# Kernel optimization log

Hardware: AMD Instinct MI355X
Metric: run time of the kernel (lower is better)

The kernel has to match this reference:

```python
import jax, jax.numpy as jnp
import numpy as np

B, S, D, H, DFF = 2, 2048, 1024, 16, 4096
DH = D // H
EPS = 1e-8


def _alibi_bias(num_heads, seq_len, dtype=jnp.float32):
    # ALiBi slopes for power-of-two head counts: 2^(-8*(h+1)/H)
    h = jnp.arange(1, num_heads + 1, dtype=dtype)
    slopes = jnp.exp2(-8.0 * h / num_heads)          # [H]
    pos = jnp.arange(seq_len, dtype=dtype)
    rel = jnp.abs(pos[None, :] - pos[:, None])       # [S, S] |i-j|
    return -slopes[:, None, None] * rel[None]        # [H, S, S]


def _rmsnorm(x, scale):
    rms = jax.lax.rsqrt(jnp.mean(x * x, axis=-1, keepdims=True) + EPS)
    return scale * x * rms


def setup_inputs() -> dict:
    key = jax.random.key(0)
    ks = jax.random.split(key, 12)
    sd = 0.02
    return {
        "x": jax.random.normal(ks[0], (B, S, D), jnp.float32),
        "scale1": jnp.ones((D,), jnp.float32),
        "scale2": jnp.ones((D,), jnp.float32),
        "w_qkv": jax.random.normal(ks[1], (D, 3 * D), jnp.float32) * sd,
        "b_qkv": jnp.zeros((3 * D,), jnp.float32),
        "w_out": jax.random.normal(ks[2], (D, D), jnp.float32) * sd,
        "b_out": jnp.zeros((D,), jnp.float32),
        "w1": jax.random.normal(ks[3], (D, DFF), jnp.float32) * sd,
        "b1": jnp.zeros((DFF,), jnp.float32),
        "w2": jax.random.normal(ks[4], (DFF, D), jnp.float32) * sd,
        "b2": jnp.zeros((D,), jnp.float32),
    }


def reference(x, scale1, scale2, w_qkv, b_qkv, w_out, b_out, w1, b1, w2, b2):
    residual = x
    xn = _rmsnorm(x, scale1)
    qkv = xn @ w_qkv + b_qkv                                  # [B,S,3D]
    q, k, v = jnp.split(qkv, 3, axis=-1)
    def heads(t):
        return t.reshape(B, S, H, DH).transpose(0, 2, 1, 3)   # [B,H,S,DH]
    q, k, v = heads(q), heads(k), heads(v)
    scores = jnp.einsum("bhsd,bhtd->bhst", q, k) / (DH ** 0.5)
    scores = scores + _alibi_bias(H, S, scores.dtype)[None]
    attn = jax.nn.softmax(scores, axis=-1)
    out = jnp.einsum("bhst,bhtd->bhsd", attn, v)              # [B,H,S,DH]
    out = out.transpose(0, 2, 1, 3).reshape(B, S, D)
    x = residual + (out @ w_out + b_out)
    residual = x
    xn = _rmsnorm(x, scale2)
    h = jax.nn.gelu(xn @ w1 + b1, approximate=False)
    return residual + (h @ w2 + b2)
```

## Files before the change

### kernel.cpp

```cpp
#include <hip/hip_runtime.h>
#include <hip/hip_bf16.h>
#include <math.h>

#define B_ 2
#define S_ 2048
#define D_ 1024
#define H_ 16
#define DH_ 64
#define DFF_ 4096
#define M_ (B_*S_)

typedef __bf16 bf16;
typedef __bf16 bf16x8 __attribute__((ext_vector_type(8)));
typedef __bf16 bf16x4 __attribute__((ext_vector_type(4)));
typedef float f32x4 __attribute__((ext_vector_type(4)));

__device__ __forceinline__ void gll16(const void* g, void* l) {
  __builtin_amdgcn_global_load_lds(
      (const __attribute__((address_space(1))) void*)g,
      (__attribute__((address_space(3))) void*)l, 16, 0, 0);
}

#define WAITCNT_VM4 0xF74
#define WAITCNT_VM0 0xF70

__global__ __launch_bounds__(256) void rmsnorm_kernel(const float* __restrict__ x,
    const float* __restrict__ scale, bf16* __restrict__ out) {
  __shared__ float red[4];
  int row = blockIdx.x, t = threadIdx.x;
  const float4* xr = (const float4*)(x + (size_t)row * D_);
  float4 v = xr[t];
  float ss = v.x*v.x + v.y*v.y + v.z*v.z + v.w*v.w;
  #pragma unroll
  for (int off = 32; off > 0; off >>= 1) ss += __shfl_down(ss, off, 64);
  if ((t & 63) == 0) red[t >> 6] = ss;
  __syncthreads();
  float tot = red[0] + red[1] + red[2] + red[3];
  float r = rsqrtf(tot * (1.0f / D_) + 1e-8f);
  float4 sc = ((const float4*)scale)[t];
  bf16x4 o;
  o[0] = (bf16)(v.x * sc.x * r);
  o[1] = (bf16)(v.y * sc.y * r);
  o[2] = (bf16)(v.z * sc.z * r);
  o[3] = (bf16)(v.w * sc.w * r);
  *(bf16x4*)(out + (size_t)row * D_ + t * 4) = o;
}

__global__ __launch_bounds__(256) void reduce_rms_kernel(
    const bf16* __restrict__ p0, const bf16* __restrict__ p1,
    const float* __restrict__ x, const float* __restrict__ bias,
    const float* __restrict__ scale, float* __restrict__ x2, bf16* __restrict__ xn2) {
  __shared__ float red[4];
  int row = blockIdx.x, t = threadIdx.x;
  float4 xv = ((const float4*)(x + (size_t)row * D_))[t];
  float4 bv = ((const float4*)bias)[t];
  bf16x4 a = *(const bf16x4*)(p0 + (size_t)row * D_ + t * 4);
  bf16x4 b = *(const bf16x4*)(p1 + (size_t)row * D_ + t * 4);
  float s0 = xv.x + bv.x + (float)a[0] + (float)b[0];
  float s1 = xv.y + bv.y + (float)a[1] + (float)b[1];
  float s2 = xv.z + bv.z + (float)a[2] + (float)b[2];
  float s3 = xv.w + bv.w + (float)a[3] + (float)b[3];
  float4 o; o.x = s0; o.y = s1; o.z = s2; o.w = s3;
  ((float4*)(x2 + (size_t)row * D_))[t] = o;
  float ss = s0*s0 + s1*s1 + s2*s2 + s3*s3;
  #pragma unroll
  for (int off = 32; off > 0; off >>= 1) ss += __shfl_down(ss, off, 64);
  if ((t & 63) == 0) red[t >> 6] = ss;
  __syncthreads();
  float tot = red[0] + red[1] + red[2] + red[3];
  float r = rsqrtf(tot * (1.0f / D_) + 1e-8f);
  float4 sc = ((const float4*)scale)[t];
  bf16x4 on;
  on[0] = (bf16)(s0 * sc.x * r);
  on[1] = (bf16)(s1 * sc.y * r);
  on[2] = (bf16)(s2 * sc.z * r);
  on[3] = (bf16)(s3 * sc.w * r);
  *(bf16x4*)(xn2 + (size_t)row * D_ + t * 4) = on;
}

__global__ __launch_bounds__(256) void reduce_out_kernel(
    const bf16* __restrict__ p0, const bf16* __restrict__ p1,
    const float* __restrict__ x2, const float* __restrict__ bias,
    float* __restrict__ dout) {
  int row = blockIdx.x, t = threadIdx.x;
  float4 xv = ((const float4*)(x2 + (size_t)row * D_))[t];
  float4 bv = ((const float4*)bias)[t];
  bf16x4 a = *(const bf16x4*)(p0 + (size_t)row * D_ + t * 4);
  bf16x4 b = *(const bf16x4*)(p1 + (size_t)row * D_ + t * 4);
  float4 o;
  o.x = xv.x + bv.x + (float)a[0] + (float)b[0];
  o.y = xv.y + bv.y + (float)a[1] + (float)b[1];
  o.z = xv.z + bv.z + (float)a[2] + (float)b[2];
  o.w = xv.w + bv.w + (float)a[3] + (float)b[3];
  ((float4*)(dout + (size_t)row * D_))[t] = o;
}

__global__ __launch_bounds__(256) void wtrans_kernel(const float* __restrict__ W,
    bf16* __restrict__ Wt, int K, int N) {
  __shared__ float tile[32][33];
  int n0 = blockIdx.x * 32, k0 = blockIdx.y * 32;
  int tx = threadIdx.x & 31, ty = threadIdx.x >> 5;
  #pragma unroll
  for (int i = 0; i < 4; i++)
    tile[ty + i*8][tx] = W[(size_t)(k0 + ty + i*8) * N + n0 + tx];
  __syncthreads();
  #pragma unroll
  for (int i = 0; i < 4; i++)
    Wt[(size_t)(n0 + ty + i*8) * K + k0 + tx] = (bf16)tile[tx][ty + i*8];
}

__global__ __launch_bounds__(256) void vtrans_kernel(const bf16* __restrict__ Vin,
    bf16* __restrict__ Vt) {
  __shared__ bf16 tile[32][34];
  size_t base = (size_t)blockIdx.z * (S_ * DH_);
  int s0 = blockIdx.x * 32, d0 = blockIdx.y * 32;
  int tx = threadIdx.x & 31, ty = threadIdx.x >> 5;
  #pragma unroll
  for (int i = 0; i < 4; i++)
    tile[ty + i*8][tx] = Vin[base + (size_t)(s0 + ty + i*8) * DH_ + d0 + tx];
  __syncthreads();
  #pragma unroll
  for (int i = 0; i < 4; i++)
    Vt[base + (size_t)(d0 + ty + i*8) * S_ + s0 + tx] = tile[tx][ty + i*8];
}

__device__ __forceinline__ float gelu_fast(float x) {
  float e = __builtin_amdgcn_exp2f(2.3022585093f * x * (1.0f + 0.044715f * x * x));
  return x * e / (1.0f + e);
}

template<int MODE>
__global__ __launch_bounds__(256) void gemm_kernel(
    const bf16* __restrict__ A, const bf16* __restrict__ Bt,
    const float* __restrict__ bias, void* __restrict__ outp, void* __restrict__ outp2,
    int M, int N, int K, int lda) {
  __shared__ __align__(16) bf16 As[3][128 * 32];
  __shared__ __align__(16) bf16 Bs[3][128 * 32];
  int t = threadIdx.x;
  int wave = t >> 6, lane = t & 63;
  int lm = lane & 15, lg = lane >> 4;
  int m0 = blockIdx.y * 128, n0 = blockIdx.x * 128;
  size_t koff = (size_t)blockIdx.z * K;
  int wm = (wave >> 1) * 64, wn = (wave & 1) * 64;
  f32x4 acc[4][4] = {};

  int srow = t >> 2, sslot = t & 3;
  int scol = (sslot ^ ((srow >> 1) & 3)) * 8;
  const bf16* Ag = A + (size_t)(m0 + srow) * lda + koff + scol;
  const bf16* Bg = Bt + (size_t)(n0 + srow) * lda + koff + scol;
  size_t half = (size_t)64 * lda;
  int rsw = (lm >> 1) & 3;
  int nk = K >> 5;

  gll16(Ag, As[0] + t * 8);
  gll16(Ag + half, As[0] + 2048 + t * 8);
  gll16(Bg, Bs[0] + t * 8);
  gll16(Bg + half, Bs[0] + 2048 + t * 8);
  if (nk > 1) {
    gll16(Ag + 32, As[1] + t * 8);
    gll16(Ag + 32 + half, As[1] + 2048 + t * 8);
    gll16(Bg + 32, Bs[1] + t * 8);
    gll16(Bg + 32 + half, Bs[1] + 2048 + t * 8);
  }

  int buf = 0;
  for (int j = 0; j < nk; ++j) {
    if (j + 1 < nk) __builtin_amdgcn_s_waitcnt(WAITCNT_VM4);
    else            __builtin_amdgcn_s_waitcnt(WAITCNT_VM0);
    __builtin_amdgcn_s_barrier();
    if (j + 2 < nk) {
      int k2 = (j + 2) << 5;
      int nbuf = buf + 2; if (nbuf >= 3) nbuf -= 3;
      bf16* Ad = As[nbuf];
      bf16* Bd = Bs[nbuf];
      gll16(Ag + k2, Ad + t * 8);
      gll16(Ag + k2 + half, Ad + 2048 + t * 8);
      gll16(Bg + k2, Bd + t * 8);
      gll16(Bg + k2 + half, Bd + 2048 + t * 8);
    }
    const bf16* Ab = As[buf];
    const bf16* Bb = Bs[buf];
    if (++buf == 3) buf = 0;
    bf16x8 af[4], bfr[4];
    #pragma unroll
    for (int i = 0; i < 4; i++)
      af[i] = *(const bf16x8*)(Ab + (wm + i * 16 + lm) * 32 + (lg ^ rsw) * 8);
    #pragma unroll
    for (int j2 = 0; j2 < 4; j2++)
      bfr[j2] = *(const bf16x8*)(Bb + (wn + j2 * 16 + lm) * 32 + (lg ^ rsw) * 8);
    #pragma unroll
    for (int i = 0; i < 4; i++)
      #pragma unroll
      for (int j2 = 0; j2 < 4; j2++)
        acc[i][j2] = __builtin_amdgcn_mfma_f32_16x16x32_bf16(af[i], bfr[j2], acc[i][j2], 0, 0, 0);
  }

  bf16* pout = (MODE == 5) ? ((blockIdx.z == 0) ? (bf16*)outp : (bf16*)outp2) : (bf16*)outp;

  #pragma unroll
  for (int i = 0; i < 4; i++) {
    int row = m0 + wm + i * 16 + lg * 4;
    #pragma unroll
    for (int j = 0; j < 4; j++) {
      int col = n0 + wn + j * 16 + lm;
      float bcol = (MODE == 5) ? 0.f : bias[col];
      #pragma unroll
      for (int r = 0; r < 4; r++) {
        float v = acc[i][j][r] + bcol;
        int rr = row + r;
        if (MODE == 0) {
          int which = col >> 10, d = col & 1023;
          int hh = d >> 6, dh = d & 63;
          int bb = rr >> 11, s = rr & 2047;
          ((bf16*)outp)[(size_t)which * ((size_t)B_*H_*S_*DH_) +
              ((size_t)(bb * H_ + hh) * S_ + s) * DH_ + dh] = (bf16)v;
        } else if (MODE == 2) {
          ((bf16*)outp)[(size_t)rr * N + col] = (bf16)gelu_fast(v);
        } else {
          pout[(size_t)rr * N + col] = (bf16)v;
        }
      }
    }
  }
}

#define PSTR 68
__global__ __launch_bounds__(256, 3) void attn_kernel(
    const bf16* __restrict__ q, const bf16* __restrict__ k,
    const bf16* __restrict__ vT, bf16* __restrict__ ao) {
  __shared__ __align__(16) bf16 Ks[2][64 * 64];
  __shared__ __align__(16) bf16 Vs[2][64 * 64];
  __shared__ __align__(16) bf16 Ps[4 * 16 * PSTR];
  int t = threadIdx.x, wave = t >> 6, lane = t & 63;
  int lm = lane & 15, lg = lane >> 4;
  int q0 = blockIdx.x * 64;
  int h = blockIdx.y, b = blockIdx.z;
  size_t base = (size_t)(b * H_ + h) * ((size_t)S_ * DH_);
  const bf16* Q = q + base;
  const bf16* K = k + base;
  const bf16* V = vT + base;
  const float LOG2E = 1.4426950408889634f;
  float sl2 = exp2f(-0.5f * (float)(h + 1)) * LOG2E;
  float nslope = -sl2;
  const float qscale = 0.125f * LOG2E;
  const float FMAX = 8.0f;

  int W = (int)(24.0f / sl2);
  int jlo = (q0 - W) >> 6; if (jlo < 0) jlo = 0;
  int jhi = ((q0 + 63 + W) >> 6) + 1; if (jhi > S_ / 64) jhi = S_ / 64;

  bf16x8 qf[2];
  #pragma unroll
  for (int h2 = 0; h2 < 2; h2++) {
    bf16x8 v = *(const bf16x8*)(Q + (size_t)(q0 + wave * 16 + lm) * DH_ + h2 * 32 + lg * 8);
    #pragma unroll
    for (int e = 0; e < 8; e++) v[e] = (bf16)((float)v[e] * qscale);
    qf[h2] = v;
  }

  int row0 = t >> 3, jslot = t & 7;
  int gsw = (jslot ^ (row0 & 7)) << 3;
  const bf16* Ksrc0 = K + (size_t)row0 * DH_ + gsw;
  const bf16* Vsrc0 = V + (size_t)row0 * S_ + gsw;

  {
    int jt = jlo << 6;
    gll16(Ksrc0 + (size_t)jt * DH_, Ks[0] + (size_t)t * 8);
    gll16(Ksrc0 + (size_t)(jt + 32) * DH_, Ks[0] + (size_t)(t + 256) * 8);
    gll16(Vsrc0 + jt, Vs[0] + (size_t)t * 8);
    gll16(Vsrc0 + (size_t)32 * S_ + jt, Vs[0] + (size_t)(t + 256) * 8);
  }

  f32x4 oacc[4] = {};
  float rs[4] = {0.f, 0.f, 0.f, 0.f};
  int psw = lm & 7;

  for (int jj = jlo; jj < jhi; ++jj) {
    int buf = (jj - jlo) & 1;
    int jt = jj << 6;
    __syncthreads();
    if (jj + 1 < jhi) {
      int jn = (jj + 1) << 6;
      gll16(Ksrc0 + (size_t)jn * DH_, Ks[buf ^ 1] + (size_t)t * 8);
      gll16(Ksrc0 + (size_t)(jn + 32) * DH_, Ks[buf ^ 1] + (size_t)(t + 256) * 8);
      gll16(Vsrc0 + jn, Vs[buf ^ 1] + (size_t)t * 8);
      gll16(Vsrc0 + (size_t)32 * S_ + jn, Vs[buf ^ 1] + (size_t)(t + 256) * 8);
    }
    const bf16* Kb = Ks[buf];
    const bf16* Vb = Vs[buf];

    f32x4 sc[4];
    #pragma unroll
    for (int tt = 0; tt < 4; tt++) {
      f32x4 a = {-FMAX, -FMAX, -FMAX, -FMAX};
      int krow = tt * 16 + lm;
      bf16x8 kb0 = *(const bf16x8*)(Kb + (size_t)(krow * 8 + (lg ^ psw)) * 8);
      bf16x8 kb1 = *(const bf16x8*)(Kb + (size_t)(krow * 8 + ((lg + 4) ^ psw)) * 8);
      a = __builtin_amdgcn_mfma_f32_16x16x32_bf16(qf[0], kb0, a, 0, 0, 0);
      a = __builtin_amdgcn_mfma_f32_16x16x32_bf16(qf[1], kb1, a, 0, 0, 0);
      sc[tt] = a;
    }

    bf16* Pw = Ps + wave * (16 * PSTR);
    int i0 = q0 + wave * 16 + lg * 4;
    #pragma unroll
    for (int tt = 0; tt < 4; tt++) {
      float f0 = (float)(i0 - jt - tt * 16 - lm);
      #pragma unroll
      for (int r = 0; r < 4; r++) {
        float s2 = fmaf(nslope, fabsf(f0 + (float)r), sc[tt][r]);
        float p = __builtin_amdgcn_exp2f(s2);
        rs[r] += p;
        Pw[(lg * 4 + r) * PSTR + tt * 16 + lm] = (bf16)p;
      }
    }

    bf16x8 ap0 = *(const bf16x8*)(Pw + lm * PSTR + lg * 8);
    bf16x8 ap1 = *(const bf16x8*)(Pw + lm * PSTR + 32 + lg * 8);
    #pragma unroll
    for (int tt = 0; tt < 4; tt++) {
      int vrow = tt * 16 + lm;
      bf16x8 vb0 = *(const bf16x8*)(Vb + (size_t)(vrow * 8 + (lg ^ psw)) * 8);
      bf16x8 vb1 = *(const bf16x8*)(Vb + (size_t)(vrow * 8 + ((lg + 4) ^ psw)) * 8);
      oacc[tt] = __builtin_amdgcn_mfma_f32_16x16x32_bf16(ap0, vb0, oacc[tt], 0, 0, 0);
      oacc[tt] = __builtin_amdgcn_mfma_f32_16x16x32_bf16(ap1, vb1, oacc[tt], 0, 0, 0);
    }
  }

  #pragma unroll
  for (int r = 0; r < 4; r++) {
    #pragma unroll
    for (int off = 1; off < 16; off <<= 1)
      rs[r] += __shfl_xor(rs[r], off, 16);
  }

  #pragma unroll
  for (int r = 0; r < 4; r++) {
    float inv = 1.0f / rs[r];
    int row = q0 + wave * 16 + lg * 4 + r;
    #pragma unroll
    for (int tt = 0; tt < 4; tt++) {
      int col = h * 64 + tt * 16 + lm;
      ao[((size_t)(b * S_) + row) * D_ + col] = (bf16)(oacc[tt][r] * inv);
    }
  }
}

extern "C" void kernel_launch(void* const* d_in, const int* in_sizes, int n_in,
                              void* d_out, int out_size, void* d_ws, size_t ws_size,
                              hipStream_t stream) {
  const float* x      = (const float*)d_in[0];
  const float* scale1 = (const float*)d_in[1];
  const float* scale2 = (const float*)d_in[2];
  const float* w_qkv  = (const float*)d_in[3];
  const float* b_qkv  = (const float*)d_in[4];
  const float* w_out  = (const float*)d_in[5];
  const float* b_out  = (const float*)d_in[6];
  const float* w1     = (const float*)d_in[7];
  const float* b1     = (const float*)d_in[8];
  const float* w2     = (const float*)d_in[9];
  const float* b2     = (const float*)d_in[10];

  char* ws = (char*)d_ws;
  const size_t MB = 1024 * 1024;
  bf16* xn    = (bf16*)(ws + 0);
  bf16* qb    = (bf16*)(ws + 8*MB);
  bf16* kb    = (bf16*)(ws + 16*MB);
  bf16* vb    = (bf16*)(ws + 24*MB);
  bf16* vT    = (bf16*)(ws + 32*MB);
  bf16* wqkvT = (bf16*)(ws + 40*MB);
  bf16* woutT = (bf16*)(ws + 46*MB);
  bf16* w1T   = (bf16*)(ws + 48*MB);
  bf16* w2T   = (bf16*)(ws + 56*MB);
  float* x2   = (float*)(ws + 64*MB);
  bf16* xn2   = qb;
  bf16* pp0   = kb;
  bf16* pp1   = vb;
  bf16* hbuf  = kb;
  bf16* qp0   = xn;
  bf16* qp1   = w1T;
  bf16* ao    = xn;

  dim3 blk(256);
  wtrans_kernel<<<dim3(3072/32, 1024/32), blk, 0, stream>>>(w_qkv, wqkvT, 1024, 3072);
  wtrans_kernel<<<dim3(1024/32, 1024/32), blk, 0, stream>>>(w_out, woutT, 1024, 1024);
  wtrans_kernel<<<dim3(4096/32, 1024/32), blk, 0, stream>>>(w1, w1T, 1024, 4096);
  wtrans_kernel<<<dim3(1024/32, 4096/32), blk, 0, stream>>>(w2, w2T, 4096, 1024);

  rmsnorm_kernel<<<dim3(M_), blk, 0, stream>>>(x, scale1, xn);

  gemm_kernel<0><<<dim3(3072/128, M_/128, 1), blk, 0, stream>>>(
      xn, wqkvT, b_qkv, qb, nullptr, M_, 3072, 1024, 1024);

  vtrans_kernel<<<dim3(S_/32, DH_/32, B_*H_), blk, 0, stream>>>(vb, vT);

  attn_kernel<<<dim3(S_/64, H_, B_), blk, 0, stream>>>(qb, kb, vT, ao);

  gemm_kernel<5><<<dim3(1024/128, M_/128, 2), blk, 0, stream>>>(
      ao, woutT, nullptr, pp0, pp1, M_, 1024, 512, 1024);
  reduce_rms_kernel<<<dim3(M_), blk, 0, stream>>>(pp0, pp1, x, b_out, scale2, x2, xn2);

  gemm_kernel<2><<<dim3(4096/128, M_/128, 1), blk, 0, stream>>>(
      xn2, w1T, b1, hbuf, nullptr, M_, 4096, 1024, 1024);

  gemm_kernel<5><<<dim3(1024/128, M_/128, 2), blk, 0, stream>>>(
      hbuf, w2T, nullptr, qp0, qp1, M_, 1024, 2048, 4096);
  reduce_out_kernel<<<dim3(M_), blk, 0, stream>>>(qp0, qp1, x2, b2, (float*)d_out);
}
```

Baseline: 373.6 us.

## Split attention KV range across two blocks and add a combine kernel

```diff
diff --git a/kernel.cpp b/kernel.cpp
--- a/kernel.cpp
+++ b/kernel.cpp
@@ -227,14 +227,15 @@
 #define PSTR 68
 __global__ __launch_bounds__(256, 3) void attn_kernel(
     const bf16* __restrict__ q, const bf16* __restrict__ k,
-    const bf16* __restrict__ vT, bf16* __restrict__ ao) {
+    const bf16* __restrict__ vT, bf16* __restrict__ pbuf, float* __restrict__ rsbuf) {
   __shared__ __align__(16) bf16 Ks[2][64 * 64];
   __shared__ __align__(16) bf16 Vs[2][64 * 64];
   __shared__ __align__(16) bf16 Ps[4 * 16 * PSTR];
   int t = threadIdx.x, wave = t >> 6, lane = t & 63;
   int lm = lane & 15, lg = lane >> 4;
-  int q0 = blockIdx.x * 64;
-  int h = blockIdx.y, b = blockIdx.z;
+  int qt = blockIdx.x, q0 = qt * 64;
+  int h = 15 - blockIdx.y;
+  int b = blockIdx.z >> 1, c = blockIdx.z & 1;
   size_t base = (size_t)(b * H_ + h) * ((size_t)S_ * DH_);
   const bf16* Q = q + base;
   const bf16* K = k + base;
@@ -248,6 +249,20 @@
   int W = (int)(24.0f / sl2);
   int jlo = (q0 - W) >> 6; if (jlo < 0) jlo = 0;
   int jhi = ((q0 + 63 + W) >> 6) + 1; if (jhi > S_ / 64) jhi = S_ / 64;
+  int n = jhi - jlo, nc0 = (n + 1) >> 1;
+  int cjlo = c ? jlo + nc0 : jlo;
+  int cjhi = c ? jhi : jlo + nc0;
+  int slot = ((b * H_ + h) * 32 + qt) * 2 + c;
+  bf16* Pout = pbuf + (size_t)slot * 4096;
+  float* Rout = rsbuf + (size_t)slot * 64;
+
+  if (cjlo >= cjhi) {
+    uint4 z = {0, 0, 0, 0};
+    *(uint4*)(Pout + t * 8) = z;
+    *(uint4*)(Pout + 2048 + t * 8) = z;
+    if (t < 64) Rout[t] = 0.f;
+    return;
+  }
 
   bf16x8 qf[2];
   #pragma unroll
@@ -264,7 +279,7 @@
   const bf16* Vsrc0 = V + (size_t)row0 * S_ + gsw;
 
   {
-    int jt = jlo << 6;
+    int jt = cjlo << 6;
     gll16(Ksrc0 + (size_t)jt * DH_, Ks[0] + (size_t)t * 8);
     gll16(Ksrc0 + (size_t)(jt + 32) * DH_, Ks[0] + (size_t)(t + 256) * 8);
     gll16(Vsrc0 + jt, Vs[0] + (size_t)t * 8);
@@ -275,11 +290,11 @@
   float rs[4] = {0.f, 0.f, 0.f, 0.f};
   int psw = lm & 7;
 
-  for (int jj = jlo; jj < jhi; ++jj) {
-    int buf = (jj - jlo) & 1;
+  for (int jj = cjlo; jj < cjhi; ++jj) {
+    int buf = (jj - cjlo) & 1;
     int jt = jj << 6;
     __syncthreads();
-    if (jj + 1 < jhi) {
+    if (jj + 1 < cjhi) {
       int jn = (jj + 1) << 6;
       gll16(Ksrc0 + (size_t)jn * DH_, Ks[buf ^ 1] + (size_t)t * 8);
       gll16(Ksrc0 + (size_t)(jn + 32) * DH_, Ks[buf ^ 1] + (size_t)(t + 256) * 8);
@@ -336,14 +351,35 @@
 
   #pragma unroll
   for (int r = 0; r < 4; r++) {
-    float inv = 1.0f / rs[r];
-    int row = q0 + wave * 16 + lg * 4 + r;
-    #pragma unroll
-    for (int tt = 0; tt < 4; tt++) {
-      int col = h * 64 + tt * 16 + lm;
-      ao[((size_t)(b * S_) + row) * D_ + col] = (bf16)(oacc[tt][r] * inv);
-    }
-  }
+    int lrow = wave * 16 + lg * 4 + r;
+    if (lm == 0) Rout[lrow] = rs[r];
+    #pragma unroll
+    for (int tt = 0; tt < 4; tt++)
+      Pout[lrow * 64 + tt * 16 + lm] = (bf16)oacc[tt][r];
+  }
+}
+
+__global__ __launch_bounds__(256) void attn_combine_kernel(
+    const bf16* __restrict__ pbuf, const float* __restrict__ rsbuf,
+    bf16* __restrict__ ao) {
+  int qt = blockIdx.x, h = blockIdx.y, b = blockIdx.z;
+  int slot0 = ((b * H_ + h) * 32 + qt) * 2;
+  int t = threadIdx.x;
+  int row = t >> 2, cg = (t & 3) * 16;
+  const bf16* P0 = pbuf + (size_t)slot0 * 4096 + row * 64 + cg;
+  const bf16* P1 = pbuf + (size_t)(slot0 + 1) * 4096 + row * 64 + cg;
+  float inv = 1.0f / (rsbuf[(size_t)slot0 * 64 + row] + rsbuf[(size_t)(slot0 + 1) * 64 + row]);
+  bf16x8 a0 = *(const bf16x8*)P0, a1 = *(const bf16x8*)(P0 + 8);
+  bf16x8 b0 = *(const bf16x8*)P1, b1 = *(const bf16x8*)(P1 + 8);
+  bf16x8 o0, o1;
+  #pragma unroll
+  for (int e = 0; e < 8; e++) {
+    o0[e] = (bf16)(((float)a0[e] + (float)b0[e]) * inv);
+    o1[e] = (bf16)(((float)a1[e] + (float)b1[e]) * inv);
+  }
+  bf16* dst = ao + ((size_t)(b * S_) + qt * 64 + row) * D_ + h * 64 + cg;
+  *(bf16x8*)dst = o0;
+  *(bf16x8*)(dst + 8) = o1;
 }
 
 extern "C" void kernel_launch(void* const* d_in, const int* in_sizes, int n_in,
@@ -380,6 +416,8 @@
   bf16* qp0   = xn;
   bf16* qp1   = w1T;
   bf16* ao    = xn;
+  bf16* pbuf  = (bf16*)(ws + 64*MB);
+  float* rsbuf = (float*)(ws + 40*MB);
 
   dim3 blk(256);
   wtrans_kernel<<<dim3(3072/32, 1024/32), blk, 0, stream>>>(w_qkv, wqkvT, 1024, 3072);
@@ -394,7 +432,8 @@
 
   vtrans_kernel<<<dim3(S_/32, DH_/32, B_*H_), blk, 0, stream>>>(vb, vT);
 
-  attn_kernel<<<dim3(S_/64, H_, B_), blk, 0, stream>>>(qb, kb, vT, ao);
+  attn_kernel<<<dim3(S_/64, H_, B_*2), blk, 0, stream>>>(qb, kb, vT, pbuf, rsbuf);
+  attn_combine_kernel<<<dim3(S_/64, H_, B_), blk, 0, stream>>>(pbuf, rsbuf, ao);
 
   gemm_kernel<5><<<dim3(1024/128, M_/128, 2), blk, 0, stream>>>(
       ao, woutT, nullptr, pp0, pp1, M_, 1024, 512, 1024);
```

New measurement: 371.2 us. No clear change (-0.6%).
